# Performance work log

Hardware: AMD Instinct MI355X
Metric: run time of the kernel (lower is better)

## Reference

```python
import jax, jax.numpy as jnp
import numpy as np

B, T, D = 4, 2048, 1024
H = 16
HD = D // H

def setup_inputs() -> dict:
    key = jax.random.key(0)
    ks = jax.random.split(key, 3)
    x = jax.random.normal(ks[0], (B, T, D), dtype=jnp.float32)
    w_qkv = jax.random.normal(ks[1], (D, 3 * D), dtype=jnp.float32) * (1.0 / np.sqrt(D))
    b_qkv = jnp.zeros((3 * D,), dtype=jnp.float32)
    w_proj = jax.random.normal(ks[2], (D, D), dtype=jnp.float32) * (1.0 / np.sqrt(D))
    b_proj = jnp.zeros((D,), dtype=jnp.float32)
    return {"x": x, "w_qkv": w_qkv, "b_qkv": b_qkv, "w_proj": w_proj, "b_proj": b_proj}

def reference(x, w_qkv, b_qkv, w_proj, b_proj):
    b, t, c = x.shape
    qkv = x @ w_qkv + b_qkv                      # [B,T,3D]
    qkv = qkv.reshape(b, t, 3, H, HD).transpose(2, 0, 3, 1, 4)  # [3,B,H,T,HD]
    q, k, v = qkv[0], qkv[1], qkv[2]
    scale = jnp.sqrt(jnp.asarray(HD, dtype=x.dtype))
    attn = jnp.einsum('bhqd,bhkd->bhqk', q, k) / scale  # [B,H,T,T]
    causal = jnp.tril(jnp.ones((t, t), dtype=bool))
    attn = jnp.where(causal[None, None], attn, -jnp.inf)
    attn = jax.nn.softmax(attn, axis=-1)
    out = jnp.einsum('bhqk,bhkd->bhqd', attn, v)        # [B,H,T,HD]
    out = out.transpose(0, 2, 1, 3).reshape(b, t, c)
    return out @ w_proj + b_proj
```

## Files before the change

kernel.cpp:

```cpp
#include <hip/hip_runtime.h>

typedef float f32x4 __attribute__((ext_vector_type(4)));
typedef __bf16 bf16x8 __attribute__((ext_vector_type(8)));

static __device__ __forceinline__ unsigned short f2bf(float f) {
    unsigned int u = __builtin_bit_cast(unsigned int, f);
    u += 0x7fffu + ((u >> 16) & 1u);
    return (unsigned short)(u >> 16);
}
static __device__ __forceinline__ unsigned short bfc(float f) {
    return __builtin_bit_cast(unsigned short, (__bf16)f);
}

#define QSC 0.18033688011112042f

typedef const __attribute__((address_space(1))) unsigned int gu32;
typedef __attribute__((address_space(3))) unsigned int lu32;
static __device__ __forceinline__ void gload_lds16(const unsigned short* g, unsigned short* l) {
    __builtin_amdgcn_global_load_lds((gu32*)g, (lu32*)l, 16, 0, 0);
}

__global__ __launch_bounds__(256)
void cvt_bf16(const float* __restrict__ in, unsigned short* __restrict__ out) {
    int i = blockIdx.x * 256 + threadIdx.x;
    const float4* p = (const float4*)in + (size_t)i * 2;
    float4 a = p[0], b = p[1];
    union { unsigned short s[8]; uint4 v; } u;
    u.s[0] = f2bf(a.x); u.s[1] = f2bf(a.y); u.s[2] = f2bf(a.z); u.s[3] = f2bf(a.w);
    u.s[4] = f2bf(b.x); u.s[5] = f2bf(b.y); u.s[6] = f2bf(b.z); u.s[7] = f2bf(b.w);
    ((uint4*)out)[i] = u.v;
}

__global__ __launch_bounds__(256)
void transpose_w(const float* __restrict__ w, unsigned short* __restrict__ wT,
                 int K, int N) {
    __shared__ unsigned short Lt[64][65];
    const int k0 = blockIdx.x * 64, n0 = blockIdx.y * 64;
    const int t = threadIdx.x;
    const int r = t >> 4, c4 = (t & 15) * 4;
    #pragma unroll
    for (int i = 0; i < 4; i++) {
        int rr = r + i * 16;
        float4 v = *(const float4*)(w + (k0 + rr) * N + n0 + c4);
        Lt[rr][c4 + 0] = f2bf(v.x); Lt[rr][c4 + 1] = f2bf(v.y);
        Lt[rr][c4 + 2] = f2bf(v.z); Lt[rr][c4 + 3] = f2bf(v.w);
    }
    __syncthreads();
    const int rn = t >> 3, ks = (t & 7) * 8;
    #pragma unroll
    for (int i = 0; i < 2; i++) {
        int rr = rn + i * 32;
        unsigned short tmp[8];
        #pragma unroll
        for (int j = 0; j < 8; j++) tmp[j] = Lt[ks + j][rr];
        *(uint4*)(wT + (n0 + rr) * K + k0 + ks) = *(const uint4*)tmp;
    }
}

__global__ __launch_bounds__(256)
void qkv_gemm2(const unsigned short* __restrict__ A,
               const unsigned short* __restrict__ Bt,
               const float* __restrict__ bias,
               unsigned short* __restrict__ q_ws,
               unsigned short* __restrict__ k_ws,
               unsigned short* __restrict__ vT_ws)
{
    const int K = 1024;
    __shared__ unsigned short Al[2][128 * 32];
    __shared__ unsigned short Bl[2][128 * 32];
    const int tid = threadIdx.x;
    const int lane = tid & 63, w = tid >> 6;
    const int l15 = lane & 15, lhi = lane >> 4;
    const int m0 = blockIdx.x * 128, n0 = blockIdx.y * 128;
    const int wm = (w >> 1) * 64, wn = (w & 1) * 64;

    const int srow = w * 32 + (lane >> 2);
    const int sslot = lane & 3;
    const unsigned short* ga = A + (size_t)(m0 + srow) * K + sslot * 8;
    const unsigned short* gb = Bt + (size_t)(n0 + srow) * K + sslot * 8;
    const int lofs = w * 32 * 32;

    f32x4 acc[4][4] = {};

    gload_lds16(ga, &Al[0][lofs]);
    gload_lds16(ga + 16 * K, &Al[0][lofs + 512]);
    gload_lds16(gb, &Bl[0][lofs]);
    gload_lds16(gb + 16 * K, &Bl[0][lofs + 512]);
    __syncthreads();

    int cur = 0;
    for (int k0 = 0; k0 < K; k0 += 32) {
        const int nxt = cur ^ 1;
        if (k0 + 32 < K) {
            gload_lds16(ga + k0 + 32,          &Al[nxt][lofs]);
            gload_lds16(ga + k0 + 32 + 16 * K, &Al[nxt][lofs + 512]);
            gload_lds16(gb + k0 + 32,          &Bl[nxt][lofs]);
            gload_lds16(gb + k0 + 32 + 16 * K, &Bl[nxt][lofs + 512]);
        }
        bf16x8 af[4], bfr[4];
        #pragma unroll
        for (int m = 0; m < 4; m++)
            af[m] = *(const bf16x8*)(&Al[cur][(wm + m * 16 + l15) * 32 + lhi * 8]);
        #pragma unroll
        for (int n = 0; n < 4; n++)
            bfr[n] = *(const bf16x8*)(&Bl[cur][(wn + n * 16 + l15) * 32 + lhi * 8]);
        __builtin_amdgcn_s_setprio(1);
        #pragma unroll
        for (int m = 0; m < 4; m++)
            #pragma unroll
            for (int n = 0; n < 4; n++)
                acc[m][n] = __builtin_amdgcn_mfma_f32_16x16x32_bf16(af[m], bfr[n], acc[m][n], 0, 0, 0);
        __builtin_amdgcn_s_setprio(0);
        __syncthreads();
        cur = nxt;
    }

    #pragma unroll
    for (int n = 0; n < 4; n++) {
        int col = n0 + wn + n * 16 + l15;
        float bv = bias[col];
        int which = col >> 10;
        int d = col & 1023;
        int h = d >> 6, hd = d & 63;
        #pragma unroll
        for (int m = 0; m < 4; m++) {
            #pragma unroll
            for (int j = 0; j < 4; j++) {
                int row = m0 + wm + m * 16 + lhi * 4 + j;
                int b = row >> 11, t = row & 2047;
                float val = acc[m][n][j] + bv;
                int bh = b * 16 + h;
                if (which == 0)      q_ws[(bh * 2048 + t) * 64 + hd] = f2bf(val * QSC);
                else if (which == 1) k_ws[(bh * 2048 + t) * 64 + hd] = f2bf(val);
                else                 vT_ws[(bh * 64 + hd) * 2048 + t] = f2bf(val);
            }
        }
    }
}

#define LKK 72

__global__ __launch_bounds__(512, 4)
void attn_fwd(const unsigned short* __restrict__ q_ws,
              const unsigned short* __restrict__ k_ws,
              const unsigned short* __restrict__ vT_ws,
              unsigned short* __restrict__ attn_ws)
{
    __shared__ unsigned short Kb[2][64 * LKK];
    __shared__ unsigned short Vb[2][64 * LKK];
    __shared__ unsigned short Pl[8][16 * 64];

    const int bh = blockIdx.x;
    const int p  = blockIdx.y;
    const int b = bh >> 4, h = bh & 15;
    const int tid = threadIdx.x;
    const int lane = tid & 63, wid = tid >> 6;
    const int l15 = lane & 15, lhi = lane >> 4;
    const int tbase = bh * 2048;
    const float NINF = -__builtin_inff();

    const int r0 = tid >> 3;
    const int c0 = (tid & 7) * 8;
    const unsigned short* kg = k_ws + (size_t)(tbase + r0) * 64 + c0;
    const unsigned short* vg = vT_ws + ((size_t)bh * 64 + r0) * 2048 + c0;

    unsigned short* Pw = &Pl[wid][0];
    const int xr = l15 & 7;

    #pragma unroll 1
    for (int seg = 0; seg < 2; ++seg) {
        const int qb = seg ? p : 15 - p;
        const int q0 = qb * 128;
        const int qrow = q0 + wid * 16;
        const int nkv = 2 * (qb + 1);

        bf16x8 qf[2];
        #pragma unroll
        for (int ks = 0; ks < 2; ks++)
            qf[ks] = *(const bf16x8*)(q_ws + (size_t)(tbase + qrow + l15) * 64 + ks * 32 + lhi * 8);

        f32x4 o[4] = {};
        float mreg = NINF, lst = 0.f;

        {
            uint4 ka = *(const uint4*)(kg);
            uint4 va = *(const uint4*)(vg);
            *(uint4*)(&Kb[0][r0 * LKK + c0]) = ka;
            *(uint4*)(&Vb[0][r0 * LKK + c0]) = va;
        }
        __syncthreads();

        int cur = 0;
        for (int kb = 0; kb < nkv; ++kb) {
            const int k0 = kb * 64;
            const int knx = (kb + 1 < nkv ? kb + 1 : kb) * 64;
            uint4 ka = *(const uint4*)(kg + (size_t)knx * 64);
            uint4 va = *(const uint4*)(vg + knx);

            if (k0 <= qrow + 15) {
                f32x4 s[4] = {};
                __builtin_amdgcn_s_setprio(1);
                #pragma unroll
                for (int ks = 0; ks < 2; ks++) {
                    bf16x8 kf[4];
                    #pragma unroll
                    for (int n = 0; n < 4; n++)
                        kf[n] = *(const bf16x8*)(&Kb[cur][(n * 16 + l15) * LKK + ks * 32 + lhi * 8]);
                    #pragma unroll
                    for (int n = 0; n < 4; n++)
                        s[n] = __builtin_amdgcn_mfma_f32_16x16x32_bf16(kf[n], qf[ks], s[n], 0, 0, 0);
                }
                __builtin_amdgcn_s_setprio(0);
                if (k0 + 63 > qrow) {
                    int qg = qrow + l15;
                    #pragma unroll
                    for (int n = 0; n < 4; n++) {
                        int kgl = k0 + n * 16 + lhi * 4;
                        #pragma unroll
                        for (int j = 0; j < 4; j++)
                            s[n][j] = (kgl + j <= qg) ? s[n][j] : NINF;
                    }
                }
                float mx = NINF;
                #pragma unroll
                for (int n = 0; n < 4; n++)
                    #pragma unroll
                    for (int j = 0; j < 4; j++)
                        mx = fmaxf(mx, s[n][j]);
                mx = fmaxf(mx, __shfl_xor(mx, 16));
                mx = fmaxf(mx, __shfl_xor(mx, 32));

                if (__all(mx <= mreg + 8.f)) {
                    float rs = 0.f;
                    #pragma unroll
                    for (int n = 0; n < 4; n++)
                        #pragma unroll
                        for (int j = 0; j < 4; j++) {
                            float pv = exp2f(s[n][j] - mreg);
                            s[n][j] = pv;
                            rs += pv;
                        }
                    rs += __shfl_xor(rs, 16);
                    rs += __shfl_xor(rs, 32);
                    lst += rs;
                } else {
                    float mnew = fmaxf(mreg, mx);
                    float al = exp2f(mreg - mnew);
                    mreg = mnew;
                    float rs = 0.f;
                    #pragma unroll
                    for (int n = 0; n < 4; n++)
                        #pragma unroll
                        for (int j = 0; j < 4; j++) {
                            float pv = exp2f(s[n][j] - mnew);
                            s[n][j] = pv;
                            rs += pv;
                        }
                    rs += __shfl_xor(rs, 16);
                    rs += __shfl_xor(rs, 32);
                    lst = lst * al + rs;
                    #pragma unroll
                    for (int j = 0; j < 4; j++) {
                        float a = __shfl(al, lhi * 4 + j);
                        #pragma unroll
                        for (int nd = 0; nd < 4; nd++)
                            o[nd][j] *= a;
                    }
                }
                #pragma unroll
                for (int n = 0; n < 4; n++) {
                    ushort4 pk;
                    pk.x = bfc(s[n][0]); pk.y = bfc(s[n][1]);
                    pk.z = bfc(s[n][2]); pk.w = bfc(s[n][3]);
                    int chunk = (2 * n + (lhi >> 1)) ^ xr;
                    *(ushort4*)(&Pw[l15 * 64 + chunk * 8 + (lhi & 1) * 4]) = pk;
                }
                __builtin_amdgcn_s_setprio(1);
                #pragma unroll
                for (int ks = 0; ks < 2; ks++) {
                    int chunk = (4 * ks + lhi) ^ xr;
                    bf16x8 pf = *(const bf16x8*)(&Pw[l15 * 64 + chunk * 8]);
                    bf16x8 vf[4];
                    #pragma unroll
                    for (int nd = 0; nd < 4; nd++)
                        vf[nd] = *(const bf16x8*)(&Vb[cur][(nd * 16 + l15) * LKK + ks * 32 + lhi * 8]);
                    #pragma unroll
                    for (int nd = 0; nd < 4; nd++)
                        o[nd] = __builtin_amdgcn_mfma_f32_16x16x32_bf16(pf, vf[nd], o[nd], 0, 0, 0);
                }
                __builtin_amdgcn_s_setprio(0);
            }
            *(uint4*)(&Kb[cur ^ 1][r0 * LKK + c0]) = ka;
            *(uint4*)(&Vb[cur ^ 1][r0 * LKK + c0]) = va;
            __syncthreads();
            cur ^= 1;
        }
        #pragma unroll
        for (int j = 0; j < 4; j++) {
            float lv = __shfl(lst, lhi * 4 + j);
            float inv = 1.0f / lv;
            int t = qrow + lhi * 4 + j;
            #pragma unroll
            for (int nd = 0; nd < 4; nd++) {
                int d = nd * 16 + l15;
                attn_ws[((size_t)(b * 2048 + t) * 16 + h) * 64 + d] = f2bf(o[nd][j] * inv);
            }
        }
    }
}

__global__ __launch_bounds__(256)
void proj_gemm2(const unsigned short* __restrict__ A,
                const unsigned short* __restrict__ Bt,
                const float* __restrict__ bias, float* __restrict__ out)
{
    const int K = 1024, N = 1024;
    __shared__ unsigned short Al[2][128 * 32];
    __shared__ unsigned short Bl[2][128 * 32];
    const int tid = threadIdx.x;
    const int lane = tid & 63, w = tid >> 6;
    const int l15 = lane & 15, lhi = lane >> 4;
    const int m0 = blockIdx.x * 128, n0 = blockIdx.y * 128;
    const int wm = (w >> 1) * 64, wn = (w & 1) * 64;

    const int srow = w * 32 + (lane >> 2);
    const int sslot = lane & 3;
    const unsigned short* ga = A + (size_t)(m0 + srow) * K + sslot * 8;
    const unsigned short* gb = Bt + (size_t)(n0 + srow) * K + sslot * 8;
    const int lofs = w * 32 * 32;

    f32x4 acc[4][4] = {};

    gload_lds16(ga, &Al[0][lofs]);
    gload_lds16(ga + 16 * K, &Al[0][lofs + 512]);
    gload_lds16(gb, &Bl[0][lofs]);
    gload_lds16(gb + 16 * K, &Bl[0][lofs + 512]);
    __syncthreads();

    int cur = 0;
    for (int k0 = 0; k0 < K; k0 += 32) {
        const int nxt = cur ^ 1;
        if (k0 + 32 < K) {
            gload_lds16(ga + k0 + 32,          &Al[nxt][lofs]);
            gload_lds16(ga + k0 + 32 + 16 * K, &Al[nxt][lofs + 512]);
            gload_lds16(gb + k0 + 32,          &Bl[nxt][lofs]);
            gload_lds16(gb + k0 + 32 + 16 * K, &Bl[nxt][lofs + 512]);
        }
        bf16x8 af[4], bfr[4];
        #pragma unroll
        for (int m = 0; m < 4; m++)
            af[m] = *(const bf16x8*)(&Al[cur][(wm + m * 16 + l15) * 32 + lhi * 8]);
        #pragma unroll
        for (int n = 0; n < 4; n++)
            bfr[n] = *(const bf16x8*)(&Bl[cur][(wn + n * 16 + l15) * 32 + lhi * 8]);
        __builtin_amdgcn_s_setprio(1);
        #pragma unroll
        for (int m = 0; m < 4; m++)
            #pragma unroll
            for (int n = 0; n < 4; n++)
                acc[m][n] = __builtin_amdgcn_mfma_f32_16x16x32_bf16(af[m], bfr[n], acc[m][n], 0, 0, 0);
        __builtin_amdgcn_s_setprio(0);
        __syncthreads();
        cur = nxt;
    }

    #pragma unroll
    for (int n = 0; n < 4; n++) {
        int col = n0 + wn + n * 16 + l15;
        float bv = bias[col];
        #pragma unroll
        for (int m = 0; m < 4; m++)
            #pragma unroll
            for (int j = 0; j < 4; j++) {
                int row = m0 + wm + m * 16 + lhi * 4 + j;
                out[row * N + col] = acc[m][n][j] + bv;
            }
    }
}

extern "C" void kernel_launch(void* const* d_in, const int* in_sizes, int n_in,
                              void* d_out, int out_size, void* d_ws, size_t ws_size,
                              hipStream_t stream)
{
    const float* x      = (const float*)d_in[0];
    const float* w_qkv  = (const float*)d_in[1];
    const float* b_qkv  = (const float*)d_in[2];
    const float* w_proj = (const float*)d_in[3];
    const float* b_proj = (const float*)d_in[4];
    float* out = (float*)d_out;

    const size_t SEG = (size_t)8 * 1024 * 1024;
    unsigned short* q_ws    = (unsigned short*)d_ws;
    unsigned short* k_ws    = q_ws + SEG;
    unsigned short* vT_ws   = k_ws + SEG;
    unsigned short* attn_ws = vT_ws + SEG;

    unsigned short* x_bf   = (unsigned short*)d_out;
    unsigned short* wqkvT  = x_bf + SEG;
    unsigned short* wprojT = q_ws;

    cvt_bf16<<<4096, 256, 0, stream>>>(x, x_bf);
    transpose_w<<<dim3(16, 48), 256, 0, stream>>>(w_qkv, wqkvT, 1024, 3072);
    qkv_gemm2<<<dim3(64, 24), 256, 0, stream>>>(x_bf, wqkvT, b_qkv, q_ws, k_ws, vT_ws);
    attn_fwd<<<dim3(64, 8), 512, 0, stream>>>(q_ws, k_ws, vT_ws, attn_ws);
    transpose_w<<<dim3(16, 16), 256, 0, stream>>>(w_proj, wprojT, 1024, 1024);
    proj_gemm2<<<dim3(64, 8), 256, 0, stream>>>(attn_ws, wprojT, b_proj, out);
}
```

Before: 199.5 us.

## Rewrite QKV GEMM with 256x256 tiles, 8 waves, swizzled LDS and staged prefetch

Replaces the 128x128, 4-wave QKV GEMM with a 256x256-tile, 8-wave kernel that uses a K-step of 64 and XOR-swizzled LDS layouts to avoid bank conflicts. Global-to-LDS loads are split into half-tile stages and interleaved between four MFMA phases, using explicit vmcnt waits and scheduling barriers for finer overlap. The intent is more data reuse per LDS byte and better hiding of memory latency. The cost is a larger LDS footprint, more registers and fewer blocks (384) to fill the CUs.

```diff
diff --git a/kernel.cpp b/kernel.cpp
--- a/kernel.cpp
+++ b/kernel.cpp
@@ -18,6 +18,11 @@
 typedef __attribute__((address_space(3))) unsigned int lu32;
 static __device__ __forceinline__ void gload_lds16(const unsigned short* g, unsigned short* l) {
     __builtin_amdgcn_global_load_lds((gu32*)g, (lu32*)l, 16, 0, 0);
+}
+static __device__ __forceinline__ void sbar() {
+    __builtin_amdgcn_sched_barrier(0);
+    __builtin_amdgcn_s_barrier();
+    __builtin_amdgcn_sched_barrier(0);
 }
 
 __global__ __launch_bounds__(256)
@@ -57,82 +62,149 @@
     }
 }
 
-__global__ __launch_bounds__(256)
-void qkv_gemm2(const unsigned short* __restrict__ A,
+#define GK 1024
+#define NT 16
+
+__global__ __launch_bounds__(512, 2)
+void qkv_gemm3(const unsigned short* __restrict__ A,
                const unsigned short* __restrict__ Bt,
                const float* __restrict__ bias,
                unsigned short* __restrict__ q_ws,
                unsigned short* __restrict__ k_ws,
                unsigned short* __restrict__ vT_ws)
 {
-    const int K = 1024;
-    __shared__ unsigned short Al[2][128 * 32];
-    __shared__ unsigned short Bl[2][128 * 32];
+    __shared__ unsigned short L[2][2][16384];
     const int tid = threadIdx.x;
     const int lane = tid & 63, w = tid >> 6;
     const int l15 = lane & 15, lhi = lane >> 4;
-    const int m0 = blockIdx.x * 128, n0 = blockIdx.y * 128;
-    const int wm = (w >> 1) * 64, wn = (w & 1) * 64;
-
-    const int srow = w * 32 + (lane >> 2);
-    const int sslot = lane & 3;
-    const unsigned short* ga = A + (size_t)(m0 + srow) * K + sslot * 8;
-    const unsigned short* gb = Bt + (size_t)(n0 + srow) * K + sslot * 8;
-    const int lofs = w * 32 * 32;
-
-    f32x4 acc[4][4] = {};
-
-    gload_lds16(ga, &Al[0][lofs]);
-    gload_lds16(ga + 16 * K, &Al[0][lofs + 512]);
-    gload_lds16(gb, &Bl[0][lofs]);
-    gload_lds16(gb + 16 * K, &Bl[0][lofs + 512]);
-    __syncthreads();
-
-    int cur = 0;
-    for (int k0 = 0; k0 < K; k0 += 32) {
-        const int nxt = cur ^ 1;
-        if (k0 + 32 < K) {
-            gload_lds16(ga + k0 + 32,          &Al[nxt][lofs]);
-            gload_lds16(ga + k0 + 32 + 16 * K, &Al[nxt][lofs + 512]);
-            gload_lds16(gb + k0 + 32,          &Bl[nxt][lofs]);
-            gload_lds16(gb + k0 + 32 + 16 * K, &Bl[nxt][lofs + 512]);
-        }
-        bf16x8 af[4], bfr[4];
-        #pragma unroll
-        for (int m = 0; m < 4; m++)
-            af[m] = *(const bf16x8*)(&Al[cur][(wm + m * 16 + l15) * 32 + lhi * 8]);
-        #pragma unroll
-        for (int n = 0; n < 4; n++)
-            bfr[n] = *(const bf16x8*)(&Bl[cur][(wn + n * 16 + l15) * 32 + lhi * 8]);
+    const int m0 = blockIdx.x * 256, n0 = blockIdx.y * 256;
+    const int wr = w >> 2, wc = w & 3;
+
+    const int srow0 = w * 8 + (lane >> 3);
+    const int selem = ((lane & 7) * 8) ^ (((srow0 >> 1) & 3) << 3);
+    const unsigned short* gA0 = A  + (size_t)(m0 + srow0) * GK + selem;
+    const unsigned short* gB0 = Bt + (size_t)(n0 + srow0) * GK + selem;
+
+    #define STAGE(op, h, bufi, kt) do { \
+        const unsigned short* _s = ((op) ? gB0 : gA0) + (size_t)(h) * 128 * GK + (kt) * 64; \
+        unsigned short* _d = &L[bufi][op][(h) * 8192 + w * 512]; \
+        gload_lds16(_s, _d); \
+        gload_lds16(_s + 64 * GK, _d + 4096); \
+    } while (0)
+
+    const int vsw = ((l15 >> 1) & 3) << 3;
+    const int c0 = (lhi * 8) ^ vsw;
+    const int c1 = (32 + lhi * 8) ^ vsw;
+    const int arb = (wr * 128 + l15) * 64;
+    const int brb = (wc * 64 + l15) * 64;
+
+    f32x4 acc[8][4] = {};
+
+    STAGE(0, 0, 0, 0); STAGE(0, 1, 0, 0); STAGE(1, 0, 0, 0); STAGE(1, 1, 0, 0);
+    STAGE(1, 0, 1, 1); STAGE(1, 1, 1, 1);
+    asm volatile("s_waitcnt vmcnt(4)" ::: "memory");
+    sbar();
+
+    for (int t = 0; t < NT; ++t) {
+        const int buf = t & 1;
+        const unsigned short* La = &L[buf][0][0];
+        const unsigned short* Lb = &L[buf][1][0];
+        bf16x8 aq[4][2], b0q[2][2], b1q[2][2];
+
+        #pragma unroll
+        for (int f = 0; f < 4; ++f) {
+            aq[f][0] = *(const bf16x8*)&La[arb + f * 1024 + c0];
+            aq[f][1] = *(const bf16x8*)&La[arb + f * 1024 + c1];
+        }
+        #pragma unroll
+        for (int g = 0; g < 2; ++g) {
+            b1q[g][0] = *(const bf16x8*)&Lb[brb + (2 + g) * 1024 + c0];
+            b1q[g][1] = *(const bf16x8*)&Lb[brb + (2 + g) * 1024 + c1];
+        }
+        if (t + 1 < NT) STAGE(0, 0, buf ^ 1, t + 1);
+        sbar();
         __builtin_amdgcn_s_setprio(1);
         #pragma unroll
-        for (int m = 0; m < 4; m++)
-            #pragma unroll
-            for (int n = 0; n < 4; n++)
-                acc[m][n] = __builtin_amdgcn_mfma_f32_16x16x32_bf16(af[m], bfr[n], acc[m][n], 0, 0, 0);
+        for (int f = 0; f < 4; ++f)
+            #pragma unroll
+            for (int g = 0; g < 2; ++g) {
+                acc[f][2 + g] = __builtin_amdgcn_mfma_f32_16x16x32_bf16(aq[f][0], b1q[g][0], acc[f][2 + g], 0, 0, 0);
+                acc[f][2 + g] = __builtin_amdgcn_mfma_f32_16x16x32_bf16(aq[f][1], b1q[g][1], acc[f][2 + g], 0, 0, 0);
+            }
         __builtin_amdgcn_s_setprio(0);
-        __syncthreads();
-        cur = nxt;
-    }
+        sbar();
+
+        #pragma unroll
+        for (int g = 0; g < 2; ++g) {
+            b0q[g][0] = *(const bf16x8*)&Lb[brb + g * 1024 + c0];
+            b0q[g][1] = *(const bf16x8*)&Lb[brb + g * 1024 + c1];
+        }
+        if (t + 1 < NT) STAGE(0, 1, buf ^ 1, t + 1);
+        sbar();
+        __builtin_amdgcn_s_setprio(1);
+        #pragma unroll
+        for (int f = 0; f < 4; ++f)
+            #pragma unroll
+            for (int g = 0; g < 2; ++g) {
+                acc[f][g] = __builtin_amdgcn_mfma_f32_16x16x32_bf16(aq[f][0], b0q[g][0], acc[f][g], 0, 0, 0);
+                acc[f][g] = __builtin_amdgcn_mfma_f32_16x16x32_bf16(aq[f][1], b0q[g][1], acc[f][g], 0, 0, 0);
+            }
+        __builtin_amdgcn_s_setprio(0);
+        sbar();
+
+        #pragma unroll
+        for (int f = 0; f < 4; ++f) {
+            aq[f][0] = *(const bf16x8*)&La[arb + (4 + f) * 1024 + c0];
+            aq[f][1] = *(const bf16x8*)&La[arb + (4 + f) * 1024 + c1];
+        }
+        if (t + 2 < NT) STAGE(1, 0, buf, t + 2);
+        sbar();
+        __builtin_amdgcn_s_setprio(1);
+        #pragma unroll
+        for (int f = 0; f < 4; ++f)
+            #pragma unroll
+            for (int g = 0; g < 2; ++g) {
+                acc[4 + f][g] = __builtin_amdgcn_mfma_f32_16x16x32_bf16(aq[f][0], b0q[g][0], acc[4 + f][g], 0, 0, 0);
+                acc[4 + f][g] = __builtin_amdgcn_mfma_f32_16x16x32_bf16(aq[f][1], b0q[g][1], acc[4 + f][g], 0, 0, 0);
+            }
+        __builtin_amdgcn_s_setprio(0);
+        sbar();
+
+        if (t + 2 < NT) STAGE(1, 1, buf, t + 2);
+        asm volatile("s_waitcnt vmcnt(4)" ::: "memory");
+        sbar();
+        __builtin_amdgcn_s_setprio(1);
+        #pragma unroll
+        for (int f = 0; f < 4; ++f)
+            #pragma unroll
+            for (int g = 0; g < 2; ++g) {
+                acc[4 + f][2 + g] = __builtin_amdgcn_mfma_f32_16x16x32_bf16(aq[f][0], b1q[g][0], acc[4 + f][2 + g], 0, 0, 0);
+                acc[4 + f][2 + g] = __builtin_amdgcn_mfma_f32_16x16x32_bf16(aq[f][1], b1q[g][1], acc[4 + f][2 + g], 0, 0, 0);
+            }
+        __builtin_amdgcn_s_setprio(0);
+        sbar();
+    }
+    #undef STAGE
 
     #pragma unroll
-    for (int n = 0; n < 4; n++) {
-        int col = n0 + wn + n * 16 + l15;
+    for (int g = 0; g < 4; ++g) {
+        int col = n0 + wc * 64 + g * 16 + l15;
         float bv = bias[col];
         int which = col >> 10;
         int d = col & 1023;
         int h = d >> 6, hd = d & 63;
-        #pragma unroll
-        for (int m = 0; m < 4; m++) {
-            #pragma unroll
-            for (int j = 0; j < 4; j++) {
-                int row = m0 + wm + m * 16 + lhi * 4 + j;
-                int b = row >> 11, t = row & 2047;
-                float val = acc[m][n][j] + bv;
-                int bh = b * 16 + h;
-                if (which == 0)      q_ws[(bh * 2048 + t) * 64 + hd] = f2bf(val * QSC);
-                else if (which == 1) k_ws[(bh * 2048 + t) * 64 + hd] = f2bf(val);
-                else                 vT_ws[(bh * 64 + hd) * 2048 + t] = f2bf(val);
+        int bhc = h;
+        #pragma unroll
+        for (int f = 0; f < 8; ++f) {
+            #pragma unroll
+            for (int j = 0; j < 4; ++j) {
+                int row = m0 + wr * 128 + f * 16 + lhi * 4 + j;
+                int b = row >> 11, tt = row & 2047;
+                float val = acc[f][g][j] + bv;
+                int bh = b * 16 + bhc;
+                if (which == 0)      q_ws[(bh * 2048 + tt) * 64 + hd] = f2bf(val * QSC);
+                else if (which == 1) k_ws[(bh * 2048 + tt) * 64 + hd] = f2bf(val);
+                else                 vT_ws[(bh * 64 + hd) * 2048 + tt] = f2bf(val);
             }
         }
     }
@@ -401,7 +473,7 @@
 
     cvt_bf16<<<4096, 256, 0, stream>>>(x, x_bf);
     transpose_w<<<dim3(16, 48), 256, 0, stream>>>(w_qkv, wqkvT, 1024, 3072);
-    qkv_gemm2<<<dim3(64, 24), 256, 0, stream>>>(x_bf, wqkvT, b_qkv, q_ws, k_ws, vT_ws);
+    qkv_gemm3<<<dim3(32, 12), 512, 0, stream>>>(x_bf, wqkvT, b_qkv, q_ws, k_ws, vT_ws);
     attn_fwd<<<dim3(64, 8), 512, 0, stream>>>(q_ws, k_ws, vT_ws, attn_ws);
     transpose_w<<<dim3(16, 16), 256, 0, stream>>>(w_proj, wprojT, 1024, 1024);
     proj_gemm2<<<dim3(64, 8), 256, 0, stream>>>(attn_ws, wprojT, b_proj, out);
```

Result: slower. 220.8 us (+10.6%).
